# Kernel tuning notes

Hardware: AMD Instinct MI355X
Metric: run time of the kernel (lower is better)

Reference implementation:

```python
import jax, jax.numpy as jnp
import numpy as np

N_NODES = 50000
N_EDGES = 800000
IN_CH = 256
OUT_CH = 128


def setup_inputs() -> dict:
    key = jax.random.key(0)
    k1, k2, k3, k4, k5, k6 = jax.random.split(key, 6)
    x = jax.random.normal(k1, (N_NODES, IN_CH), dtype=jnp.float32)
    edge_rows = jax.random.randint(k2, (N_EDGES,), 0, N_NODES, dtype=jnp.int64)
    edge_cols = jax.random.randint(k3, (N_EDGES,), 0, N_NODES, dtype=jnp.int64)
    # positive edge weights, roughly like a normalized adjacency (~1/degree)
    edge_vals = jax.random.uniform(k4, (N_EDGES,), dtype=jnp.float32) / 16.0
    # xavier_uniform: bound = sqrt(6/(fan_in+fan_out))
    bound = float(np.sqrt(6.0 / (IN_CH + OUT_CH)))
    weight = jax.random.uniform(k5, (IN_CH, OUT_CH), dtype=jnp.float32, minval=-bound, maxval=bound)
    gate_weight = jax.random.uniform(k6, (IN_CH, OUT_CH), dtype=jnp.float32, minval=-bound, maxval=bound)
    return {"x": x, "edge_rows": edge_rows, "edge_cols": edge_cols,
            "edge_vals": edge_vals, "weight": weight, "gate_weight": gate_weight}


def _spmm(edge_rows, edge_cols, edge_vals, dense, n_rows):
    # out[r] = sum over edges (r, c, v): v * dense[c]
    gathered = edge_vals[:, None] * dense[edge_cols]  # [E, out_ch]
    return jax.ops.segment_sum(gathered, edge_rows, num_segments=n_rows)


def reference(x, edge_rows, edge_cols, edge_vals, weight, gate_weight):
    support = x @ weight          # [N, out_ch]
    gate = x @ gate_weight        # [N, out_ch]
    n = x.shape[0]
    agg_support = _spmm(edge_rows, edge_cols, edge_vals, support, n)
    agg_gate = _spmm(edge_rows, edge_cols, edge_vals, gate, n)
    return jax.nn.sigmoid(agg_gate) * agg_support
```

## Files before the change

kernel.cpp:

```cpp
#include <hip/hip_runtime.h>
#include <hip/hip_bf16.h>

#define IN_CH 256
#define OUT_CH 128
#define NCAT 256
#define CAP 64
#define RPB 128
#define BINCAP 3072
#define EPB 4096

typedef __attribute__((ext_vector_type(8))) short bf16x8;
typedef __attribute__((ext_vector_type(4))) float f32x4;

__device__ __forceinline__ unsigned short f2bf(float f) {
  unsigned int u = __builtin_bit_cast(unsigned int, f);
  u += 0x7FFFu + ((u >> 16) & 1u);
  return (unsigned short)(u >> 16);
}
__device__ __forceinline__ unsigned int pack2bf(float a, float b) {
  return (unsigned int)f2bf(a) | ((unsigned int)f2bf(b) << 16);
}
__device__ __forceinline__ float bflo(unsigned int u) {
  return __builtin_bit_cast(float, u << 16);
}
__device__ __forceinline__ float bfhi(unsigned int u) {
  return __builtin_bit_cast(float, u & 0xFFFF0000u);
}

__global__ __launch_bounds__(256) void init_wcat(
    const float* __restrict__ w, const float* __restrict__ gw,
    unsigned short* __restrict__ wcatT, int* __restrict__ coarse_cnt,
    int nbins) {
  const int b = blockIdx.x;
  if (b < 256) {
    const int c = b;
    const int k = threadIdx.x;
    const float v = (c < 128) ? w[(size_t)k * 128 + c]
                              : gw[(size_t)k * 128 + (c - 128)];
    wcatT[(size_t)c * 256 + k] = f2bf(v);
  } else {
    for (int j = threadIdx.x; j < nbins; j += 256) coarse_cnt[j] = 0;
  }
}

__global__ __launch_bounds__(256) void bin_coarse(
    const int* __restrict__ er, const int* __restrict__ ec,
    const float* __restrict__ ev, int* __restrict__ coarse_cnt,
    unsigned* __restrict__ cA, unsigned char* __restrict__ cB,
    int E, int nbins) {
  __shared__ int scnt[512];
  __shared__ int sbase[512];
  const int t = threadIdx.x;
  const int e0 = blockIdx.x * EPB;

  for (int j = t; j < 512; j += 256) scnt[j] = 0;
  __syncthreads();

  int myr[16];
#pragma unroll
  for (int i = 0; i < 16; ++i) {
    const int e = e0 + i * 256 + t;
    int r = -1;
    if (e < E) { r = er[e]; atomicAdd(&scnt[r >> 7], 1); }
    myr[i] = r;
  }
  __syncthreads();

  for (int j = t; j < nbins; j += 256) {
    sbase[j] = (scnt[j] > 0) ? atomicAdd(&coarse_cnt[j], scnt[j]) : 0;
  }
  __syncthreads();
  for (int j = t; j < 512; j += 256) scnt[j] = 0;
  __syncthreads();

#pragma unroll
  for (int i = 0; i < 16; ++i) {
    const int r = myr[i];
    if (r >= 0) {
      const int e = e0 + i * 256 + t;
      const int b = r >> 7;
      const int idx = sbase[b] + atomicAdd(&scnt[b], 1);
      if (idx < BINCAP) {
        const size_t g = (size_t)b * BINCAP + idx;
        cA[g] = ((unsigned)ec[e] << 16) | (unsigned)f2bf(ev[e]);
        cB[g] = (unsigned char)(r & (RPB - 1));
      }
    }
  }
}

__global__ __launch_bounds__(256) void bin_fine(
    const int* __restrict__ coarse_cnt, const unsigned* __restrict__ cA,
    const unsigned char* __restrict__ cB, int* __restrict__ cnt,
    unsigned* __restrict__ bucket4, int nrows) {
  __shared__ unsigned fine[RPB * CAP];
  __shared__ int lcnt[RPB];
  const int t = threadIdx.x;
  const int b = blockIdx.x;
  const int r0 = b * RPB;

  for (int j = t; j < RPB; j += 256) lcnt[j] = 0;
  __syncthreads();

  const int nE = min(coarse_cnt[b], BINCAP);
  for (int i = t; i < nE; i += 256) {
    const unsigned a = cA[(size_t)b * BINCAP + i];
    const int rl = cB[(size_t)b * BINCAP + i];
    const int idx = atomicAdd(&lcnt[rl], 1);
    if (idx < CAP) fine[rl * CAP + idx] = a;
  }
  __syncthreads();

  if (t < RPB && r0 + t < nrows) cnt[r0 + t] = min(lcnt[t], CAP);

  for (int s = t; s < RPB * CAP; s += 256) {
    const int rl = s >> 6;
    const int sl = s & 63;
    if (sl < min(lcnt[rl], CAP) && r0 + rl < nrows)
      bucket4[(size_t)(r0 + rl) * CAP + sl] = fine[s];
  }
}

#define BM 128
#define BK 64
#define LDSTRIDE 144

__global__ __launch_bounds__(512) void gemm_mfma(
    const float* __restrict__ x, const unsigned short* __restrict__ wcatT,
    char* __restrict__ comb, int nrows) {
  __shared__ char smem[55296];
  char* As = smem;
  char* Bs = smem + 18432;

  const int t = threadIdx.x;
  const int lane = t & 63;
  const int wv = t >> 6;
  const int wr = wv >> 2;
  const int wc = wv & 3;
  const int blockRow = blockIdx.x * BM;
  const int lrow = lane & 15;
  const int klane = lane >> 4;

  f32x4 acc[4][4];
#pragma unroll
  for (int m = 0; m < 4; ++m)
#pragma unroll
    for (int n = 0; n < 4; ++n) acc[m][n] = (f32x4){0.f, 0.f, 0.f, 0.f};

  const int arow = t >> 2;
  const int aseg = t & 3;
  const int agrow = blockRow + arow;
  const bool aok = (agrow < nrows);
  const float* xrow = x + (size_t)agrow * IN_CH;

  const int bc = t >> 1;
  const int bhalf = t & 1;

  for (int kt = 0; kt < IN_CH; kt += BK) {
    {
      float4 v0 = make_float4(0, 0, 0, 0), v1 = v0, v2 = v0, v3 = v0;
      if (aok) {
        const float* p = xrow + kt + aseg * 16;
        v0 = *(const float4*)(p + 0);
        v1 = *(const float4*)(p + 4);
        v2 = *(const float4*)(p + 8);
        v3 = *(const float4*)(p + 12);
      }
      uint4 pk0, pk1;
      pk0.x = pack2bf(v0.x, v0.y); pk0.y = pack2bf(v0.z, v0.w);
      pk0.z = pack2bf(v1.x, v1.y); pk0.w = pack2bf(v1.z, v1.w);
      pk1.x = pack2bf(v2.x, v2.y); pk1.y = pack2bf(v2.z, v2.w);
      pk1.z = pack2bf(v3.x, v3.y); pk1.w = pack2bf(v3.z, v3.w);
      char* dst = As + arow * LDSTRIDE + aseg * 32;
      *(uint4*)(dst + 0)  = pk0;
      *(uint4*)(dst + 16) = pk1;
    }
    {
      const char* src = (const char*)wcatT + (size_t)bc * 512 + kt * 2 + bhalf * 64;
      char* dst = Bs + bc * LDSTRIDE + bhalf * 64;
#pragma unroll
      for (int j = 0; j < 4; ++j)
        *(uint4*)(dst + j * 16) = *(const uint4*)(src + j * 16);
    }
    __syncthreads();

#pragma unroll
    for (int kk = 0; kk < 2; ++kk) {
      bf16x8 af[4], bfm[4];
#pragma unroll
      for (int m = 0; m < 4; ++m)
        af[m] = *(const bf16x8*)(As + (wr * 64 + m * 16 + lrow) * LDSTRIDE + kk * 64 + klane * 16);
#pragma unroll
      for (int n = 0; n < 4; ++n)
        bfm[n] = *(const bf16x8*)(Bs + (wc * 64 + n * 16 + lrow) * LDSTRIDE + kk * 64 + klane * 16);
#pragma unroll
      for (int m = 0; m < 4; ++m)
#pragma unroll
        for (int n = 0; n < 4; ++n)
          acc[m][n] = __builtin_amdgcn_mfma_f32_16x16x32_bf16(af[m], bfm[n], acc[m][n], 0, 0, 0);
    }
    __syncthreads();
  }

#pragma unroll
  for (int h = 0; h < 2; ++h) {
    if (wr == h) {
#pragma unroll
      for (int m = 0; m < 4; ++m) {
#pragma unroll
        for (int n = 0; n < 4; ++n) {
#pragma unroll
          for (int j = 0; j < 4; ++j) {
            const int rl = m * 16 + klane * 4 + j;
            const int gcol = wc * 64 + n * 16 + lrow;
            const int ch = gcol & 127;
            const int isg = gcol >> 7;
            const int byteoff = (ch >> 1) * 8 + isg * 4 + (ch & 1) * 2;
            *(unsigned short*)(smem + rl * 512 + byteoff) = f2bf(acc[m][n][j]);
          }
        }
      }
    }
    __syncthreads();
#pragma unroll
    for (int it = 0; it < 4; ++it) {
      const int lin = it * 512 + t;
      const int rl = lin >> 5;
      const int grow = blockRow + h * 64 + rl;
      if (grow < nrows)
        *(float4*)(comb + (size_t)grow * 512 + (lin & 31) * 16) =
            *(const float4*)(smem + lin * 16);
    }
    __syncthreads();
  }
}

__global__ __launch_bounds__(256) void spmm_fused(
    const unsigned* __restrict__ bucket4, const int* __restrict__ cnt,
    const char* __restrict__ comb, float* __restrict__ out, int nrows) {
  const int wid = (int)((blockIdx.x * 256 + threadIdx.x) >> 6);
  const int lane = threadIdx.x & 63;
  if (wid >= nrows) return;

  const int deg = min(cnt[wid], CAP);
  float s0 = 0.f, s1 = 0.f, g0 = 0.f, g1 = 0.f;

  if (deg > 0) {
    const unsigned my = bucket4[(size_t)wid * CAP + lane];
    for (int d = 0; d < deg; d += 8) {
      unsigned cj[8]; float vj[8]; uint2 q[8];
#pragma unroll
      for (int j = 0; j < 8; ++j) {
        const int dj = d + j;
        const int ds = dj < deg ? dj : deg - 1;
        const unsigned ent = (unsigned)__shfl((int)my, ds);
        cj[j] = ent >> 16;
        vj[j] = (dj < deg) ? bflo(ent) : 0.f;
      }
#pragma unroll
      for (int j = 0; j < 8; ++j)
        q[j] = *(const uint2*)(comb + (size_t)cj[j] * 512 + lane * 8);
#pragma unroll
      for (int j = 0; j < 8; ++j) {
        s0 += vj[j] * bflo(q[j].x);  s1 += vj[j] * bfhi(q[j].x);
        g0 += vj[j] * bflo(q[j].y);  g1 += vj[j] * bfhi(q[j].y);
      }
    }
  }
  const float o0 = s0 / (1.f + __expf(-g0));
  const float o1 = s1 / (1.f + __expf(-g1));
  *(float2*)&out[(size_t)wid * OUT_CH + lane * 2] = make_float2(o0, o1);
}

extern "C" void kernel_launch(void* const* d_in, const int* in_sizes, int n_in,
                              void* d_out, int out_size, void* d_ws, size_t ws_size,
                              hipStream_t stream) {
  const float* x  = (const float*)d_in[0];
  const int*   er = (const int*)d_in[1];
  const int*   ec = (const int*)d_in[2];
  const float* ev = (const float*)d_in[3];
  const float* w  = (const float*)d_in[4];
  const float* gw = (const float*)d_in[5];
  float* out = (float*)d_out;

  const int N = in_sizes[0] / IN_CH;
  const int E = in_sizes[1];
  const int nbins = (N + RPB - 1) / RPB;

  char* ws = (char*)d_ws;
  char* comb = ws;
  size_t off = (size_t)N * 512;
  unsigned short* wcatT = (unsigned short*)(ws + off);  off += 256 * 256 * 2;
  int* cnt = (int*)(ws + off);                          off += ((size_t)N * 4 + 255) & ~255ull;
  unsigned* bucket4 = (unsigned*)(ws + off);            off += (size_t)N * CAP * 4;
  int* coarse_cnt = (int*)(ws + off);                   off += ((size_t)nbins * 4 + 255) & ~255ull;
  unsigned* cA = (unsigned*)(ws + off);                 off += (size_t)nbins * BINCAP * 4;
  unsigned char* cB = (unsigned char*)(ws + off);

  init_wcat<<<257, 256, 0, stream>>>(w, gw, wcatT, coarse_cnt, nbins);

  const int p1Blocks = (E + EPB - 1) / EPB;
  bin_coarse<<<p1Blocks, 256, 0, stream>>>(er, ec, ev, coarse_cnt, cA, cB, E, nbins);

  bin_fine<<<nbins, 256, 0, stream>>>(coarse_cnt, cA, cB, cnt, bucket4, N);

  const int gemmBlocks = (N + BM - 1) / BM;
  gemm_mfma<<<gemmBlocks, 512, 0, stream>>>(x, wcatT, comb, N);

  const int blocks = (N + 3) / 4;
  spmm_fused<<<blocks, 256, 0, stream>>>(bucket4, cnt, comb, out, N);
}
```

Baseline: 117.1 us.

## Merge coarse edge binning and dense GEMM into one heterogeneous launch

Combines the coarse binning kernel and the MFMA GEMM into a single launch. The first blocks do edge binning (now 512 threads, 8 edges per thread) and the remaining blocks do the GEMM tiles. Running the two independent stages side by side removes one launch and lets the memory-bound binning overlap the compute-bound GEMM, filling idle CUs. In exchange, the binning blocks now carry the GEMM's large shared-memory allocation and 512-thread launch bounds, which may reduce their occupancy.

```diff
diff --git a/kernel.cpp b/kernel.cpp
--- a/kernel.cpp
+++ b/kernel.cpp
@@ -43,49 +43,164 @@
   }
 }
 
-__global__ __launch_bounds__(256) void bin_coarse(
+#define BM 128
+#define BK 64
+#define LDSTRIDE 144
+
+__global__ __launch_bounds__(512) void gemm_and_bin(
+    const float* __restrict__ x, const unsigned short* __restrict__ wcatT,
+    char* __restrict__ comb, int nrows,
     const int* __restrict__ er, const int* __restrict__ ec,
     const float* __restrict__ ev, int* __restrict__ coarse_cnt,
     unsigned* __restrict__ cA, unsigned char* __restrict__ cB,
-    int E, int nbins) {
-  __shared__ int scnt[512];
-  __shared__ int sbase[512];
+    int E, int nbins, int binBlocks) {
+  __shared__ char smem[55296];
+
+  if (blockIdx.x < binBlocks) {
+    int* scnt = (int*)smem;
+    int* sbase = (int*)smem + 512;
+    const int t = threadIdx.x;
+    const int e0 = blockIdx.x * EPB;
+
+    if (t < 512) scnt[t] = 0;
+    __syncthreads();
+
+    int myr[8];
+#pragma unroll
+    for (int i = 0; i < 8; ++i) {
+      const int e = e0 + i * 512 + t;
+      int r = -1;
+      if (e < E) { r = er[e]; atomicAdd(&scnt[r >> 7], 1); }
+      myr[i] = r;
+    }
+    __syncthreads();
+
+    if (t < nbins)
+      sbase[t] = (scnt[t] > 0) ? atomicAdd(&coarse_cnt[t], scnt[t]) : 0;
+    __syncthreads();
+    if (t < 512) scnt[t] = 0;
+    __syncthreads();
+
+#pragma unroll
+    for (int i = 0; i < 8; ++i) {
+      const int r = myr[i];
+      if (r >= 0) {
+        const int e = e0 + i * 512 + t;
+        const int b = r >> 7;
+        const int idx = sbase[b] + atomicAdd(&scnt[b], 1);
+        if (idx < BINCAP) {
+          const size_t g = (size_t)b * BINCAP + idx;
+          cA[g] = ((unsigned)ec[e] << 16) | (unsigned)f2bf(ev[e]);
+          cB[g] = (unsigned char)(r & (RPB - 1));
+        }
+      }
+    }
+    return;
+  }
+
+  char* As = smem;
+  char* Bs = smem + 18432;
+
   const int t = threadIdx.x;
-  const int e0 = blockIdx.x * EPB;
-
-  for (int j = t; j < 512; j += 256) scnt[j] = 0;
-  __syncthreads();
-
-  int myr[16];
-#pragma unroll
-  for (int i = 0; i < 16; ++i) {
-    const int e = e0 + i * 256 + t;
-    int r = -1;
-    if (e < E) { r = er[e]; atomicAdd(&scnt[r >> 7], 1); }
-    myr[i] = r;
-  }
-  __syncthreads();
-
-  for (int j = t; j < nbins; j += 256) {
-    sbase[j] = (scnt[j] > 0) ? atomicAdd(&coarse_cnt[j], scnt[j]) : 0;
-  }
-  __syncthreads();
-  for (int j = t; j < 512; j += 256) scnt[j] = 0;
-  __syncthreads();
-
-#pragma unroll
-  for (int i = 0; i < 16; ++i) {
-    const int r = myr[i];
-    if (r >= 0) {
-      const int e = e0 + i * 256 + t;
-      const int b = r >> 7;
-      const int idx = sbase[b] + atomicAdd(&scnt[b], 1);
-      if (idx < BINCAP) {
-        const size_t g = (size_t)b * BINCAP + idx;
-        cA[g] = ((unsigned)ec[e] << 16) | (unsigned)f2bf(ev[e]);
-        cB[g] = (unsigned char)(r & (RPB - 1));
-      }
-    }
+  const int lane = t & 63;
+  const int wv = t >> 6;
+  const int wr = wv >> 2;
+  const int wc = wv & 3;
+  const int blockRow = (blockIdx.x - binBlocks) * BM;
+  const int lrow = lane & 15;
+  const int klane = lane >> 4;
+
+  f32x4 acc[4][4];
+#pragma unroll
+  for (int m = 0; m < 4; ++m)
+#pragma unroll
+    for (int n = 0; n < 4; ++n) acc[m][n] = (f32x4){0.f, 0.f, 0.f, 0.f};
+
+  const int arow = t >> 2;
+  const int aseg = t & 3;
+  const int agrow = blockRow + arow;
+  const bool aok = (agrow < nrows);
+  const float* xrow = x + (size_t)agrow * IN_CH;
+
+  const int bc = t >> 1;
+  const int bhalf = t & 1;
+
+  for (int kt = 0; kt < IN_CH; kt += BK) {
+    {
+      float4 v0 = make_float4(0, 0, 0, 0), v1 = v0, v2 = v0, v3 = v0;
+      if (aok) {
+        const float* p = xrow + kt + aseg * 16;
+        v0 = *(const float4*)(p + 0);
+        v1 = *(const float4*)(p + 4);
+        v2 = *(const float4*)(p + 8);
+        v3 = *(const float4*)(p + 12);
+      }
+      uint4 pk0, pk1;
+      pk0.x = pack2bf(v0.x, v0.y); pk0.y = pack2bf(v0.z, v0.w);
+      pk0.z = pack2bf(v1.x, v1.y); pk0.w = pack2bf(v1.z, v1.w);
+      pk1.x = pack2bf(v2.x, v2.y); pk1.y = pack2bf(v2.z, v2.w);
+      pk1.z = pack2bf(v3.x, v3.y); pk1.w = pack2bf(v3.z, v3.w);
+      char* dst = As + arow * LDSTRIDE + aseg * 32;
+      *(uint4*)(dst + 0)  = pk0;
+      *(uint4*)(dst + 16) = pk1;
+    }
+    {
+      const char* src = (const char*)wcatT + (size_t)bc * 512 + kt * 2 + bhalf * 64;
+      char* dst = Bs + bc * LDSTRIDE + bhalf * 64;
+#pragma unroll
+      for (int j = 0; j < 4; ++j)
+        *(uint4*)(dst + j * 16) = *(const uint4*)(src + j * 16);
+    }
+    __syncthreads();
+
+#pragma unroll
+    for (int kk = 0; kk < 2; ++kk) {
+      bf16x8 af[4], bfm[4];
+#pragma unroll
+      for (int m = 0; m < 4; ++m)
+        af[m] = *(const bf16x8*)(As + (wr * 64 + m * 16 + lrow) * LDSTRIDE + kk * 64 + klane * 16);
+#pragma unroll
+      for (int n = 0; n < 4; ++n)
+        bfm[n] = *(const bf16x8*)(Bs + (wc * 64 + n * 16 + lrow) * LDSTRIDE + kk * 64 + klane * 16);
+#pragma unroll
+      for (int m = 0; m < 4; ++m)
+#pragma unroll
+        for (int n = 0; n < 4; ++n)
+          acc[m][n] = __builtin_amdgcn_mfma_f32_16x16x32_bf16(af[m], bfm[n], acc[m][n], 0, 0, 0);
+    }
+    __syncthreads();
+  }
+
+#pragma unroll
+  for (int h = 0; h < 2; ++h) {
+    if (wr == h) {
+#pragma unroll
+      for (int m = 0; m < 4; ++m) {
+#pragma unroll
+        for (int n = 0; n < 4; ++n) {
+#pragma unroll
+          for (int j = 0; j < 4; ++j) {
+            const int rl = m * 16 + klane * 4 + j;
+            const int gcol = wc * 64 + n * 16 + lrow;
+            const int ch = gcol & 127;
+            const int isg = gcol >> 7;
+            const int byteoff = (ch >> 1) * 8 + isg * 4 + (ch & 1) * 2;
+            *(unsigned short*)(smem + rl * 512 + byteoff) = f2bf(acc[m][n][j]);
+          }
+        }
+      }
+    }
+    __syncthreads();
+#pragma unroll
+    for (int it = 0; it < 4; ++it) {
+      const int lin = it * 512 + t;
+      const int rl = lin >> 5;
+      const int grow = blockRow + h * 64 + rl;
+      if (grow < nrows)
+        *(float4*)(comb + (size_t)grow * 512 + (lin & 31) * 16) =
+            *(const float4*)(smem + lin * 16);
+    }
+    __syncthreads();
   }
 }
 
@@ -118,120 +233,6 @@
     const int sl = s & 63;
     if (sl < min(lcnt[rl], CAP) && r0 + rl < nrows)
       bucket4[(size_t)(r0 + rl) * CAP + sl] = fine[s];
-  }
-}
-
-#define BM 128
-#define BK 64
-#define LDSTRIDE 144
-
-__global__ __launch_bounds__(512) void gemm_mfma(
-    const float* __restrict__ x, const unsigned short* __restrict__ wcatT,
-    char* __restrict__ comb, int nrows) {
-  __shared__ char smem[55296];
-  char* As = smem;
-  char* Bs = smem + 18432;
-
-  const int t = threadIdx.x;
-  const int lane = t & 63;
-  const int wv = t >> 6;
-  const int wr = wv >> 2;
-  const int wc = wv & 3;
-  const int blockRow = blockIdx.x * BM;
-  const int lrow = lane & 15;
-  const int klane = lane >> 4;
-
-  f32x4 acc[4][4];
-#pragma unroll
-  for (int m = 0; m < 4; ++m)
-#pragma unroll
-    for (int n = 0; n < 4; ++n) acc[m][n] = (f32x4){0.f, 0.f, 0.f, 0.f};
-
-  const int arow = t >> 2;
-  const int aseg = t & 3;
-  const int agrow = blockRow + arow;
-  const bool aok = (agrow < nrows);
-  const float* xrow = x + (size_t)agrow * IN_CH;
-
-  const int bc = t >> 1;
-  const int bhalf = t & 1;
-
-  for (int kt = 0; kt < IN_CH; kt += BK) {
-    {
-      float4 v0 = make_float4(0, 0, 0, 0), v1 = v0, v2 = v0, v3 = v0;
-      if (aok) {
-        const float* p = xrow + kt + aseg * 16;
-        v0 = *(const float4*)(p + 0);
-        v1 = *(const float4*)(p + 4);
-        v2 = *(const float4*)(p + 8);
-        v3 = *(const float4*)(p + 12);
-      }
-      uint4 pk0, pk1;
-      pk0.x = pack2bf(v0.x, v0.y); pk0.y = pack2bf(v0.z, v0.w);
-      pk0.z = pack2bf(v1.x, v1.y); pk0.w = pack2bf(v1.z, v1.w);
-      pk1.x = pack2bf(v2.x, v2.y); pk1.y = pack2bf(v2.z, v2.w);
-      pk1.z = pack2bf(v3.x, v3.y); pk1.w = pack2bf(v3.z, v3.w);
-      char* dst = As + arow * LDSTRIDE + aseg * 32;
-      *(uint4*)(dst + 0)  = pk0;
-      *(uint4*)(dst + 16) = pk1;
-    }
-    {
-      const char* src = (const char*)wcatT + (size_t)bc * 512 + kt * 2 + bhalf * 64;
-      char* dst = Bs + bc * LDSTRIDE + bhalf * 64;
-#pragma unroll
-      for (int j = 0; j < 4; ++j)
-        *(uint4*)(dst + j * 16) = *(const uint4*)(src + j * 16);
-    }
-    __syncthreads();
-
-#pragma unroll
-    for (int kk = 0; kk < 2; ++kk) {
-      bf16x8 af[4], bfm[4];
-#pragma unroll
-      for (int m = 0; m < 4; ++m)
-        af[m] = *(const bf16x8*)(As + (wr * 64 + m * 16 + lrow) * LDSTRIDE + kk * 64 + klane * 16);
-#pragma unroll
-      for (int n = 0; n < 4; ++n)
-        bfm[n] = *(const bf16x8*)(Bs + (wc * 64 + n * 16 + lrow) * LDSTRIDE + kk * 64 + klane * 16);
-#pragma unroll
-      for (int m = 0; m < 4; ++m)
-#pragma unroll
-        for (int n = 0; n < 4; ++n)
-          acc[m][n] = __builtin_amdgcn_mfma_f32_16x16x32_bf16(af[m], bfm[n], acc[m][n], 0, 0, 0);
-    }
-    __syncthreads();
-  }
-
-#pragma unroll
-  for (int h = 0; h < 2; ++h) {
-    if (wr == h) {
-#pragma unroll
-      for (int m = 0; m < 4; ++m) {
-#pragma unroll
-        for (int n = 0; n < 4; ++n) {
-#pragma unroll
-          for (int j = 0; j < 4; ++j) {
-            const int rl = m * 16 + klane * 4 + j;
-            const int gcol = wc * 64 + n * 16 + lrow;
-            const int ch = gcol & 127;
-            const int isg = gcol >> 7;
-            const int byteoff = (ch >> 1) * 8 + isg * 4 + (ch & 1) * 2;
-            *(unsigned short*)(smem + rl * 512 + byteoff) = f2bf(acc[m][n][j]);
-          }
-        }
-      }
-    }
-    __syncthreads();
-#pragma unroll
-    for (int it = 0; it < 4; ++it) {
-      const int lin = it * 512 + t;
-      const int rl = lin >> 5;
-      const int grow = blockRow + h * 64 + rl;
-      if (grow < nrows)
-        *(float4*)(comb + (size_t)grow * 512 + (lin & 31) * 16) =
-            *(const float4*)(smem + lin * 16);
-    }
-    __syncthreads();
   }
 }
 
@@ -299,13 +300,12 @@
 
   init_wcat<<<257, 256, 0, stream>>>(w, gw, wcatT, coarse_cnt, nbins);
 
-  const int p1Blocks = (E + EPB - 1) / EPB;
-  bin_coarse<<<p1Blocks, 256, 0, stream>>>(er, ec, ev, coarse_cnt, cA, cB, E, nbins);
+  const int binBlocks = (E + EPB - 1) / EPB;
+  const int gemmBlocks = (N + BM - 1) / BM;
+  gemm_and_bin<<<binBlocks + gemmBlocks, 512, 0, stream>>>(
+      x, wcatT, comb, N, er, ec, ev, coarse_cnt, cA, cB, E, nbins, binBlocks);
 
   bin_fine<<<nbins, 256, 0, stream>>>(coarse_cnt, cA, cB, cnt, bucket4, N);
-
-  const int gemmBlocks = (N + BM - 1) / BM;
-  gemm_mfma<<<gemmBlocks, 512, 0, stream>>>(x, wcatT, comb, N);
 
   const int blocks = (N + 3) / 4;
   spmm_fused<<<blocks, 256, 0, stream>>>(bucket4, cnt, comb, out, N);
```

Result: faster. 109.7 us (-6.3%).
